# Kernel optimization log

Measured on AMD Instinct MI355X. Metric: run time of the kernel, lower is better.

Reference implementation:

```python
import jax, jax.numpy as jnp
import numpy as np

IN, OUT, SPLIT = 4096, 4096, 1024

def setup_inputs() -> dict:
    key = jax.random.key(0)
    ks = jax.random.split(key, 15)
    def n(k, shape, scale=0.02):
        return jax.random.normal(k, shape, dtype=jnp.float32) * scale
    inp = {
        'x':   jax.random.normal(ks[0], (4, 2048, IN), dtype=jnp.float32),
        'V':   n(ks[1], (SPLIT, IN)),
        'U':   n(ks[2], (OUT, SPLIT)),
        'v2':  n(ks[3], (1, IN), 1.0),
        'v1':  n(ks[4], (1, SPLIT), 1.0),
        'u2':  n(ks[5], (1, SPLIT), 1.0),
        'u1':  n(ks[6], (1, OUT), 1.0),
        'V_R': n(ks[7], (SPLIT, IN)),
        'U_R': n(ks[8], (OUT, SPLIT)),
        'v2_R': n(ks[9], (1, IN), 1.0),
        'v1_R': n(ks[10], (1, SPLIT), 1.0),
        'u2_R': n(ks[11], (1, SPLIT), 1.0),
        'u1_R': n(ks[12], (1, OUT), 1.0),
        'bias': n(ks[13], (OUT,), 1.0),
    }
    return inp

def _branch(xf, V, U, v2, v1, u2, u1):
    # quantize (binarize) the two low-rank factors
    Vq = jnp.sign(V)  # [split, in]
    Uq = jnp.sign(U)  # [out, split]
    # y = ((x * v2) @ Vq.T) * (v1*u2) @ Uq.T * u1
    h = (xf * v2) @ Vq.T          # [N, split]
    h = h * (v1 * u2)             # [N, split]
    return (h @ Uq.T) * u1        # [N, out]

def reference(x, V, U, v2, v1, u2, u1, V_R, U_R, v2_R, v1_R, u2_R, u1_R, bias):
    *lead, hidden = x.shape
    xf = x.reshape(-1, hidden)
    y = _branch(xf, V, U, v2, v1, u2, u1)
    y = y + _branch(xf, V_R, U_R, v2_R, v1_R, u2_R, u1_R)
    y = y + bias
    return y.reshape(*lead, -1)
```

## Files before the change

### kernel.cpp

```cpp
#include <hip/hip_runtime.h>
#include <hip/hip_bf16.h>
#include <stdint.h>


typedef __bf16 bf16x8 __attribute__((ext_vector_type(8)));
typedef float f32x4 __attribute__((ext_vector_type(4)));

__device__ __forceinline__ void async_copy16(const void* g, void* l) {
  __builtin_amdgcn_global_load_lds(
      (const __attribute__((address_space(1))) uint32_t*)g,
      (__attribute__((address_space(3))) uint32_t*)l,
      16, 0, 0);
}

__device__ __forceinline__ float sgn(float v) {
  return (v > 0.f) ? 1.f : ((v < 0.f) ? -1.f : 0.f);
}

__device__ __forceinline__ void store_out(float* p, float v) { *p = v; }
__device__ __forceinline__ void store_out(__hip_bfloat16* p, float v) { *p = __float2bfloat16(v); }

__global__ __launch_bounds__(256) void convert_x(const float* __restrict__ x,
                                                 __hip_bfloat16* __restrict__ xb,
                                                 int n) {
  int i = (blockIdx.x * 256 + threadIdx.x) * 8;
  if (i >= n) return;
  const float4* p0 = (const float4*)(x + i);
  float4 a = p0[0], b = p0[1];
  __hip_bfloat16 o[8] = {
      __float2bfloat16(a.x), __float2bfloat16(a.y), __float2bfloat16(a.z), __float2bfloat16(a.w),
      __float2bfloat16(b.x), __float2bfloat16(b.y), __float2bfloat16(b.z), __float2bfloat16(b.w)};
  *(uint4*)(xb + i) = *(const uint4*)o;
}

__global__ __launch_bounds__(256) void prep_w1(
    const float* __restrict__ V, const float* __restrict__ v2,
    const float* __restrict__ v1, const float* __restrict__ u2,
    const float* __restrict__ V_R, const float* __restrict__ v2_R,
    const float* __restrict__ v1_R, const float* __restrict__ u2_R,
    __hip_bfloat16* __restrict__ W) {
  int g = blockIdx.x * 256 + threadIdx.x;
  int k = (g & 511) * 8;
  int s = g >> 9;
  const float *Vp, *v2p;
  float rs;
  if (s < 1024) {
    Vp = V + s * 4096 + k; v2p = v2 + k; rs = v1[s] * u2[s];
  } else {
    int ss = s - 1024;
    Vp = V_R + ss * 4096 + k; v2p = v2_R + k; rs = v1_R[ss] * u2_R[ss];
  }
  __hip_bfloat16 o[8];
#pragma unroll
  for (int e = 0; e < 8; ++e)
    o[e] = __float2bfloat16(sgn(Vp[e]) * v2p[e] * rs);
  *(uint4*)(W + s * 4096 + k) = *(const uint4*)o;
}

__global__ __launch_bounds__(256) void prep_w2(
    const float* __restrict__ U, const float* __restrict__ u1,
    const float* __restrict__ U_R, const float* __restrict__ u1_R,
    __hip_bfloat16* __restrict__ W) {
  int g = blockIdx.x * 256 + threadIdx.x;
  int s = (g & 255) * 8;
  int j = g >> 8;
  const float* Up;
  float sc;
  if (s < 1024) { Up = U + j * 1024 + s;            sc = u1[j]; }
  else          { Up = U_R + j * 1024 + (s - 1024); sc = u1_R[j]; }
  __hip_bfloat16 o[8];
#pragma unroll
  for (int e = 0; e < 8; ++e)
    o[e] = __float2bfloat16(sgn(Up[e]) * sc);
  *(uint4*)(W + j * 2048 + s) = *(const uint4*)o;
}

#define PHASE(Q, BUF, LOADB, STAGE)                                            \
  {                                                                            \
    if (LOADB) {                                                               \
      _Pragma("unroll") for (int j = 0; j < 4; ++j) {                          \
        bfr[j][0] = ldb(BUF, j, 0);                                            \
        bfr[j][1] = ldb(BUF, j, 1);                                            \
      }                                                                        \
    }                                                                          \
    bf16x8 a00 = lda(BUF, 2 * (Q), 0), a01 = lda(BUF, 2 * (Q), 1);             \
    bf16x8 a10 = lda(BUF, 2 * (Q) + 1, 0), a11 = lda(BUF, 2 * (Q) + 1, 1);     \
    STAGE;                                                                     \
    asm volatile("" ::: "memory");                                             \
    __builtin_amdgcn_s_barrier();                                              \
    asm volatile("" ::: "memory");                                             \
    __builtin_amdgcn_s_setprio(1);                                             \
    _Pragma("unroll") for (int j = 0; j < 4; ++j) {                            \
      acc[2 * (Q)][j] = __builtin_amdgcn_mfma_f32_16x16x32_bf16(               \
          a00, bfr[j][0], acc[2 * (Q)][j], 0, 0, 0);                           \
      acc[2 * (Q)][j] = __builtin_amdgcn_mfma_f32_16x16x32_bf16(               \
          a01, bfr[j][1], acc[2 * (Q)][j], 0, 0, 0);                           \
      acc[2 * (Q) + 1][j] = __builtin_amdgcn_mfma_f32_16x16x32_bf16(           \
          a10, bfr[j][0], acc[2 * (Q) + 1][j], 0, 0, 0);                       \
      acc[2 * (Q) + 1][j] = __builtin_amdgcn_mfma_f32_16x16x32_bf16(           \
          a11, bfr[j][1], acc[2 * (Q) + 1][j], 0, 0, 0);                       \
    }                                                                          \
    __builtin_amdgcn_s_setprio(0);                                             \
    asm volatile("" ::: "memory");                                             \
    __builtin_amdgcn_s_barrier();                                              \
    asm volatile("" ::: "memory");                                             \
  }

template <typename OutT>
__global__ __launch_bounds__(512, 2) void gemm_bt(
    const __hip_bfloat16* __restrict__ A,
    const __hip_bfloat16* __restrict__ Bt,
    OutT* __restrict__ C,
    const float* __restrict__ bias,
    int K, int N) {
  __shared__ char smem[131072];
  const int t = threadIdx.x;
  const int lane = t & 63;
  const int w = t >> 6;
  const int wm = (w >> 2) << 7;
  const int wn = (w & 3) << 6;

  const int gx = gridDim.x;
  const int gy = gridDim.y;
  const int nwg = gx * gy;
  int lin = blockIdx.y * gx + blockIdx.x;
  {
    const int xcd = lin & 7, idx = lin >> 3, q = nwg >> 3;
    lin = xcd * q + idx;
  }
  const int grpsz = gy << 1;
  const int cg = lin / grpsz;
  const int rem = lin - cg * grpsz;
  const int bm = (rem >> 1) << 8;
  const int bn = ((cg << 1) + (rem & 1)) << 8;

  const int quad = lane >> 4;
  const int l16 = lane & 15;

  f32x4 acc[8][4] = {};
  bf16x8 bfr[4][2];

  const __hip_bfloat16* gAb = A + bm * K;
  const __hip_bfloat16* gBb = Bt + bn * K;

  auto stageA = [&](int k0, int half, int bufOff) {
#pragma unroll
    for (int r = 0; r < 2; ++r)
      async_copy16(gAb + (half * 128 + r * 64 + lane) * K + k0 + w * 8,
                   smem + bufOff + w * 4096 + half * 2048 + r * 1024 + lane * 16);
  };
  auto stageB = [&](int k0, int half, int bufOff) {
#pragma unroll
    for (int r = 0; r < 2; ++r)
      async_copy16(gBb + (half * 128 + r * 64 + lane) * K + k0 + w * 8,
                   smem + bufOff + 32768 + w * 4096 + half * 2048 + r * 1024 + lane * 16);
  };
  auto lda = [&](int bufOff, int i, int s) -> bf16x8 {
    return *(const bf16x8*)(smem + bufOff + ((s << 2) + quad) * 4096 +
                            ((wm + (i << 4) + l16) << 4));
  };
  auto ldb = [&](int bufOff, int j, int s) -> bf16x8 {
    return *(const bf16x8*)(smem + bufOff + 32768 + ((s << 2) + quad) * 4096 +
                            ((wn + (j << 4) + l16) << 4));
  };

  const int NI = K >> 7;

  stageA(0, 0, 0);
  stageA(0, 1, 0);
  stageB(0, 0, 0);
  stageB(0, 1, 0);
  stageB(64, 0, 65536);
  stageB(64, 1, 65536);
  asm volatile("s_waitcnt vmcnt(4)" ::: "memory");
  __builtin_amdgcn_s_barrier();
  asm volatile("" ::: "memory");

  for (int i = 0; i < NI; ++i) {
    const int kT = i << 7;
    const bool full = (i + 1 < NI);
    PHASE(0, 0, true,  { stageA(kT + 64, 0, 65536); })
    PHASE(1, 0, false, { stageA(kT + 64, 1, 65536); })
    PHASE(2, 0, false, { if (full) stageB(kT + 128, 0, 0); })
    PHASE(3, 0, false, {
      if (full) {
        stageB(kT + 128, 1, 0);
        asm volatile("s_waitcnt vmcnt(4)" ::: "memory");
      } else {
        asm volatile("s_waitcnt vmcnt(0)" ::: "memory");
      }
    })
    PHASE(0, 65536, true,  { if (full) stageA(kT + 128, 0, 0); })
    PHASE(1, 65536, false, { if (full) stageA(kT + 128, 1, 0); })
    PHASE(2, 65536, false, { if (full) stageB(kT + 192, 0, 65536); })
    PHASE(3, 65536, false, {
      if (full) {
        stageB(kT + 192, 1, 65536);
        asm volatile("s_waitcnt vmcnt(4)" ::: "memory");
      }
    })
  }

#pragma unroll
  for (int j = 0; j < 4; ++j) {
    int col = bn + wn + (j << 4) + l16;
    float bv = bias ? bias[col] : 0.0f;
#pragma unroll
    for (int i = 0; i < 8; ++i) {
      int row0 = bm + wm + (i << 4) + (quad << 2);
#pragma unroll
      for (int r = 0; r < 4; ++r)
        store_out(&C[(row0 + r) * N + col], acc[i][j][r] + bv);
    }
  }
}

extern "C" void kernel_launch(void* const* d_in, const int* in_sizes, int n_in,
                              void* d_out, int out_size, void* d_ws, size_t ws_size,
                              hipStream_t stream) {
  const float* x    = (const float*)d_in[0];
  const float* V    = (const float*)d_in[1];
  const float* U    = (const float*)d_in[2];
  const float* v2   = (const float*)d_in[3];
  const float* v1   = (const float*)d_in[4];
  const float* u2   = (const float*)d_in[5];
  const float* u1   = (const float*)d_in[6];
  const float* V_R  = (const float*)d_in[7];
  const float* U_R  = (const float*)d_in[8];
  const float* v2_R = (const float*)d_in[9];
  const float* v1_R = (const float*)d_in[10];
  const float* u2_R = (const float*)d_in[11];
  const float* u1_R = (const float*)d_in[12];
  const float* bias = (const float*)d_in[13];

  __hip_bfloat16* Xb  = (__hip_bfloat16*)d_ws;
  __hip_bfloat16* Wb1 = Xb + 8192 * 4096;
  __hip_bfloat16* Wb2 = Wb1 + 2048 * 4096;
  __hip_bfloat16* H   = Wb2 + 4096 * 2048;
  float* Y = (float*)d_out;

  const int nx = 8192 * 4096;
  convert_x<<<nx / (256 * 8), 256, 0, stream>>>(x, Xb, nx);
  prep_w1<<<4096, 256, 0, stream>>>(V, v2, v1, u2, V_R, v2_R, v1_R, u2_R, Wb1);
  prep_w2<<<4096, 256, 0, stream>>>(U, u1, U_R, u1_R, Wb2);

  gemm_bt<__hip_bfloat16><<<dim3(2048 / 256, 8192 / 256), 512, 0, stream>>>(
      Xb, Wb1, H, nullptr, 4096, 2048);
  gemm_bt<float><<<dim3(4096 / 256, 8192 / 256), 512, 0, stream>>>(
      H, Wb2, Y, bias, 2048, 4096);
}
```

Baseline: 582.2 us.

## Merge prep kernels into one launch and remap GEMM tiles per XCD

The three preprocessing kernels (x to bf16, W1 and W2 preparation) become a single launch whose block ranges pick the task, removing two launch gaps. The GEMM block-to-tile mapping is also changed so each XCD owns a contiguous group of N columns and walks all 32 M rows, replacing the earlier grouped swizzle. This aims at better L2 reuse of the B operand within each XCD, but the new mapping hardcodes 32 row tiles and assumes gx is divisible by 8.

```diff
diff --git a/kernel.cpp b/kernel.cpp
--- a/kernel.cpp
+++ b/kernel.cpp
@@ -20,59 +20,56 @@
 __device__ __forceinline__ void store_out(float* p, float v) { *p = v; }
 __device__ __forceinline__ void store_out(__hip_bfloat16* p, float v) { *p = __float2bfloat16(v); }
 
-__global__ __launch_bounds__(256) void convert_x(const float* __restrict__ x,
-                                                 __hip_bfloat16* __restrict__ xb,
-                                                 int n) {
-  int i = (blockIdx.x * 256 + threadIdx.x) * 8;
-  if (i >= n) return;
-  const float4* p0 = (const float4*)(x + i);
-  float4 a = p0[0], b = p0[1];
-  __hip_bfloat16 o[8] = {
-      __float2bfloat16(a.x), __float2bfloat16(a.y), __float2bfloat16(a.z), __float2bfloat16(a.w),
-      __float2bfloat16(b.x), __float2bfloat16(b.y), __float2bfloat16(b.z), __float2bfloat16(b.w)};
-  *(uint4*)(xb + i) = *(const uint4*)o;
-}
-
-__global__ __launch_bounds__(256) void prep_w1(
+__global__ __launch_bounds__(256) void prep_all(
+    const float* __restrict__ x, __hip_bfloat16* __restrict__ xb,
     const float* __restrict__ V, const float* __restrict__ v2,
     const float* __restrict__ v1, const float* __restrict__ u2,
     const float* __restrict__ V_R, const float* __restrict__ v2_R,
     const float* __restrict__ v1_R, const float* __restrict__ u2_R,
-    __hip_bfloat16* __restrict__ W) {
-  int g = blockIdx.x * 256 + threadIdx.x;
-  int k = (g & 511) * 8;
-  int s = g >> 9;
-  const float *Vp, *v2p;
-  float rs;
-  if (s < 1024) {
-    Vp = V + s * 4096 + k; v2p = v2 + k; rs = v1[s] * u2[s];
-  } else {
-    int ss = s - 1024;
-    Vp = V_R + ss * 4096 + k; v2p = v2_R + k; rs = v1_R[ss] * u2_R[ss];
-  }
-  __hip_bfloat16 o[8];
-#pragma unroll
-  for (int e = 0; e < 8; ++e)
-    o[e] = __float2bfloat16(sgn(Vp[e]) * v2p[e] * rs);
-  *(uint4*)(W + s * 4096 + k) = *(const uint4*)o;
-}
-
-__global__ __launch_bounds__(256) void prep_w2(
+    __hip_bfloat16* __restrict__ W1,
     const float* __restrict__ U, const float* __restrict__ u1,
     const float* __restrict__ U_R, const float* __restrict__ u1_R,
-    __hip_bfloat16* __restrict__ W) {
-  int g = blockIdx.x * 256 + threadIdx.x;
-  int s = (g & 255) * 8;
-  int j = g >> 8;
-  const float* Up;
-  float sc;
-  if (s < 1024) { Up = U + j * 1024 + s;            sc = u1[j]; }
-  else          { Up = U_R + j * 1024 + (s - 1024); sc = u1_R[j]; }
-  __hip_bfloat16 o[8];
-#pragma unroll
-  for (int e = 0; e < 8; ++e)
-    o[e] = __float2bfloat16(sgn(Up[e]) * sc);
-  *(uint4*)(W + j * 2048 + s) = *(const uint4*)o;
+    __hip_bfloat16* __restrict__ W2) {
+  const int b = blockIdx.x;
+  if (b < 16384) {
+    int i = (b * 256 + threadIdx.x) * 8;
+    const float4* p0 = (const float4*)(x + i);
+    float4 a = p0[0], c = p0[1];
+    __hip_bfloat16 o[8] = {
+        __float2bfloat16(a.x), __float2bfloat16(a.y), __float2bfloat16(a.z), __float2bfloat16(a.w),
+        __float2bfloat16(c.x), __float2bfloat16(c.y), __float2bfloat16(c.z), __float2bfloat16(c.w)};
+    *(uint4*)(xb + i) = *(const uint4*)o;
+  } else if (b < 20480) {
+    int g = (b - 16384) * 256 + threadIdx.x;
+    int k = (g & 511) * 8;
+    int s = g >> 9;
+    const float *Vp, *v2p;
+    float rs;
+    if (s < 1024) {
+      Vp = V + s * 4096 + k; v2p = v2 + k; rs = v1[s] * u2[s];
+    } else {
+      int ss = s - 1024;
+      Vp = V_R + ss * 4096 + k; v2p = v2_R + k; rs = v1_R[ss] * u2_R[ss];
+    }
+    __hip_bfloat16 o[8];
+#pragma unroll
+    for (int e = 0; e < 8; ++e)
+      o[e] = __float2bfloat16(sgn(Vp[e]) * v2p[e] * rs);
+    *(uint4*)(W1 + s * 4096 + k) = *(const uint4*)o;
+  } else {
+    int g = (b - 20480) * 256 + threadIdx.x;
+    int s = (g & 255) * 8;
+    int j = g >> 8;
+    const float* Up;
+    float sc;
+    if (s < 1024) { Up = U + j * 1024 + s;            sc = u1[j]; }
+    else          { Up = U_R + j * 1024 + (s - 1024); sc = u1_R[j]; }
+    __hip_bfloat16 o[8];
+#pragma unroll
+    for (int e = 0; e < 8; ++e)
+      o[e] = __float2bfloat16(sgn(Up[e]) * sc);
+    *(uint4*)(W2 + j * 2048 + s) = *(const uint4*)o;
+  }
 }
 
 #define PHASE(Q, BUF, LOADB, STAGE)                                            \
@@ -121,18 +118,14 @@
   const int wn = (w & 3) << 6;
 
   const int gx = gridDim.x;
-  const int gy = gridDim.y;
-  const int nwg = gx * gy;
   int lin = blockIdx.y * gx + blockIdx.x;
-  {
-    const int xcd = lin & 7, idx = lin >> 3, q = nwg >> 3;
-    lin = xcd * q + idx;
-  }
-  const int grpsz = gy << 1;
-  const int cg = lin / grpsz;
-  const int rem = lin - cg * grpsz;
-  const int bm = (rem >> 1) << 8;
-  const int bn = ((cg << 1) + (rem & 1)) << 8;
+  const int xcd = lin & 7;
+  const int idx = lin >> 3;
+  const int cpx = gx >> 3;
+  const int col = xcd * cpx + (idx >> 5);
+  const int row = idx & 31;
+  const int bm = row << 8;
+  const int bn = col << 8;
 
   const int quad = lane >> 4;
   const int l16 = lane & 15;
@@ -203,14 +196,14 @@
 
 #pragma unroll
   for (int j = 0; j < 4; ++j) {
-    int col = bn + wn + (j << 4) + l16;
-    float bv = bias ? bias[col] : 0.0f;
+    int col2 = bn + wn + (j << 4) + l16;
+    float bv = bias ? bias[col2] : 0.0f;
 #pragma unroll
     for (int i = 0; i < 8; ++i) {
       int row0 = bm + wm + (i << 4) + (quad << 2);
 #pragma unroll
       for (int r = 0; r < 4; ++r)
-        store_out(&C[(row0 + r) * N + col], acc[i][j][r] + bv);
+        store_out(&C[(row0 + r) * N + col2], acc[i][j][r] + bv);
     }
   }
 }
@@ -236,13 +229,11 @@
   __hip_bfloat16* Xb  = (__hip_bfloat16*)d_ws;
   __hip_bfloat16* Wb1 = Xb + 8192 * 4096;
   __hip_bfloat16* Wb2 = Wb1 + 2048 * 4096;
+  float* Y = (float*)d_out;
   __hip_bfloat16* H   = Wb2 + 4096 * 2048;
-  float* Y = (float*)d_out;
-
-  const int nx = 8192 * 4096;
-  convert_x<<<nx / (256 * 8), 256, 0, stream>>>(x, Xb, nx);
-  prep_w1<<<4096, 256, 0, stream>>>(V, v2, v1, u2, V_R, v2_R, v1_R, u2_R, Wb1);
-  prep_w2<<<4096, 256, 0, stream>>>(U, u1, U_R, u1_R, Wb2);
+
+  prep_all<<<24576, 256, 0, stream>>>(x, Xb, V, v2, v1, u2, V_R, v2_R, v1_R,
+                                      u2_R, Wb1, U, u1, U_R, u1_R, Wb2);
 
   gemm_bt<__hip_bfloat16><<<dim3(2048 / 256, 8192 / 256), 512, 0, stream>>>(
       Xb, Wb1, H, nullptr, 4096, 2048);
```

After: 588.8 us. About the same (+1.1%).
